# Optimization experiments

Measured on AMD Instinct MI355X. Metric: run time of the kernel, lower is better.

Reference implementation:

```python
import jax, jax.numpy as jnp
import numpy as np
import math

H = 1024   # d_model
NH = 32    # N // 2 state size
L_LEN = 4096
DT_MIN, DT_MAX = 0.001, 0.1


def setup_inputs() -> dict:
    key = jax.random.key(0)
    k1, k2, k3, k4 = jax.random.split(key, 4)
    C = jax.random.normal(k1, (H, NH, 2), dtype=jnp.float32)  # view_as_real complex C
    log_dt = (jax.random.uniform(k2, (H,), dtype=jnp.float32)
              * (math.log(DT_MAX) - math.log(DT_MIN)) + math.log(DT_MIN))
    # log of positive real parts (original: log(|Re(eig)|) repeated over H)
    log_A_real = jnp.log(0.5 + jax.random.uniform(k3, (H, NH), dtype=jnp.float32) * NH)
    A_imag = jax.random.normal(k4, (H, NH), dtype=jnp.float32) * math.pi
    return {"C": C, "log_dt": log_dt, "log_A_real": log_A_real,
            "A_imag": A_imag, "L": L_LEN}


def reference(C, log_dt, log_A_real, A_imag, L):
    dt = jnp.exp(log_dt)                                  # [H]
    Cc = C[..., 0] + 1j * C[..., 1]                       # [H, N] complex64
    A = -jnp.exp(log_A_real) - 1j * A_imag                # [H, N]
    dtA = A * dt[:, None]                                 # [H, N]
    # Vandermonde: exp(dtA)^l for l in [0, L)
    K = dtA[:, :, None] * jnp.arange(L, dtype=jnp.float32)  # [H, N, L]
    Cc = Cc * (jnp.exp(dtA) - 1.0) / A                    # [H, N]
    K = 2.0 * jnp.einsum('hn,hnl->hl', Cc, jnp.exp(K)).real  # [H, L]
    return K
```

## Files before the change

### kernel.cpp

```cpp
#include <hip/hip_runtime.h>
#include <math.h>


#define HH 1024
#define NH 32
#define LL 4096
#define BLOCK 256
#define CHUNK 4
#define SPLIT 4
#define STRIDE (BLOCK * SPLIT)

#define TWO_PI 6.28318530717958647692f
#define INV_TWO_PI 0.15915494309189533577f

__device__ __forceinline__ float sin_rev(float r) {
    float d;
    asm("v_sin_f32 %0, %1" : "=v"(d) : "v"(r));
    return d;
}
__device__ __forceinline__ float cos_rev(float r) {
    float d;
    asm("v_cos_f32 %0, %1" : "=v"(d) : "v"(r));
    return d;
}

__global__ __launch_bounds__(BLOCK) void s4_vandermonde(
    const float* __restrict__ C,
    const float* __restrict__ log_dt,
    const float* __restrict__ log_A_real,
    const float* __restrict__ A_imag,
    float* __restrict__ out)
{
    __shared__ float4 sA[NH];
    __shared__ float4 sB[NH];

    const int h = blockIdx.x >> 2;
    const int s = blockIdx.x & 3;
    const int t = threadIdx.x;

    if (t < NH) {
        const int n = t;
        const float dt  = __expf(log_dt[h]);
        const float Are = -__expf(log_A_real[h * NH + n]);
        const float Aim = -A_imag[h * NH + n];
        const float re = Are * dt;
        const float im = Aim * dt;
        float s1, c1;
        __sincosf(im, &s1, &c1);
        const float er1 = __expf(re);
        const float X = er1 * c1 - 1.0f;
        const float Y = er1 * s1;
        const float C0 = C[(h * NH + n) * 2 + 0];
        const float C1 = C[(h * NH + n) * 2 + 1];
        const float nr = C0 * X - C1 * Y;
        const float ni = C0 * Y + C1 * X;
        const float inv = 2.0f / (Are * Are + Aim * Aim);
        const float ctr = (nr * Are + ni * Aim) * inv;
        const float cti = (ni * Are - nr * Aim) * inv;
        const float fm = im * INV_TWO_PI;

        const float reS = re * (float)STRIDE;
        const float erS = (reS < -80.0f) ? 0.0f : __expf(reS);
        double revd = (double)fm * (double)STRIDE;
        revd -= floor(revd);
        float sS, cS;
        __sincosf((float)revd * TWO_PI, &sS, &cS);

        const float kl = -40.0f / (re * (float)STRIDE);
        const int kcap = (kl >= (float)(CHUNK - 1)) ? CHUNK : ((int)kl + 1);

        sA[n] = make_float4(ctr, cti, re, fm);
        sB[n] = make_float4(erS * cS, erS * sS, __int_as_float(kcap), 0.0f);
    }
    __syncthreads();

    float acc[CHUNK];
#pragma unroll
    for (int k = 0; k < CHUNK; ++k) acc[k] = 0.0f;

    const float lf = (float)(s * BLOCK + t);

    for (int n = 0; n < NH; ++n) {
        const float4 A4 = sA[n];
        const float a = A4.z * lf;
        if (a < -40.0f) continue;
        const float4 B4 = sB[n];
        const float er = __expf(a);
        float rev = A4.w * lf;
        rev -= floorf(rev);
        float zr = er * cos_rev(rev);
        float zi = er * sin_rev(rev);
        const int kcap = __float_as_int(B4.z);
#pragma unroll
        for (int k = 0; k < CHUNK; ++k) {
            if (k >= kcap) break;
            acc[k] += A4.x * zr - A4.y * zi;
            const float tr = zr * B4.x - zi * B4.y;
            zi = zr * B4.y + zi * B4.x;
            zr = tr;
        }
    }

    float* o = out + h * LL + s * BLOCK + t;
#pragma unroll
    for (int k = 0; k < CHUNK; ++k) o[k * STRIDE] = acc[k];
}

extern "C" void kernel_launch(void* const* d_in, const int* in_sizes, int n_in,
                              void* d_out, int out_size, void* d_ws, size_t ws_size,
                              hipStream_t stream) {
    const float* C          = (const float*)d_in[0];
    const float* log_dt     = (const float*)d_in[1];
    const float* log_A_real = (const float*)d_in[2];
    const float* A_imag     = (const float*)d_in[3];
    float* out              = (float*)d_out;

    s4_vandermonde<<<dim3(HH * SPLIT), dim3(BLOCK), 0, stream>>>(
        C, log_dt, log_A_real, A_imag, out);
}
```

Before: 86.83 us.

## Factor Vandermonde powers into shared-memory tables and use a real Chebyshev-style recurrence

Each block now precomputes per-state tables of z^e and C·z^(s*256+16e) in shared memory, using all threads, so the main loop builds z^l from one complex multiply of two table entries. This replaces the per-thread exp and sin/cos in the inner loop. The later powers at stride 1024 come from a second-order real recurrence (2Re(w)·u − |w|²·u_prev) rather than a full complex multiply. The per-n kcap early exit is replaced by a single skip threshold, and the extra barrier and table setup add a small fixed cost per block. Accuracy may drift slightly, because the factorised products and the recurrence accumulate rounding differently.

```diff
diff --git a/kernel.cpp b/kernel.cpp
--- a/kernel.cpp
+++ b/kernel.cpp
@@ -6,9 +6,8 @@
 #define NH 32
 #define LL 4096
 #define BLOCK 256
-#define CHUNK 4
 #define SPLIT 4
-#define STRIDE (BLOCK * SPLIT)
+#define STRIDE 1024
 
 #define TWO_PI 6.28318530717958647692f
 #define INV_TWO_PI 0.15915494309189533577f
@@ -31,8 +30,10 @@
     const float* __restrict__ A_imag,
     float* __restrict__ out)
 {
-    __shared__ float4 sA[NH];
-    __shared__ float4 sB[NH];
+    __shared__ float2 sW16[NH][16];
+    __shared__ float2 sW1[NH][16];
+    __shared__ float4 sP[NH];
+    __shared__ float4 sAux[NH];
 
     const int h = blockIdx.x >> 2;
     const int s = blockIdx.x & 3;
@@ -59,51 +60,71 @@
         const float cti = (ni * Are - nr * Aim) * inv;
         const float fm = im * INV_TWO_PI;
 
-        const float reS = re * (float)STRIDE;
-        const float erS = (reS < -80.0f) ? 0.0f : __expf(reS);
-        double revd = (double)fm * (double)STRIDE;
+        const float erS = __expf(re * 1024.0f);
+        double revd = (double)im * (double)INV_TWO_PI * 1024.0;
         revd -= floor(revd);
         float sS, cS;
         __sincosf((float)revd * TWO_PI, &sS, &cS);
 
-        const float kl = -40.0f / (re * (float)STRIDE);
-        const int kcap = (kl >= (float)(CHUNK - 1)) ? CHUNK : ((int)kl + 1);
-
-        sA[n] = make_float4(ctr, cti, re, fm);
-        sB[n] = make_float4(erS * cS, erS * sS, __int_as_float(kcap), 0.0f);
+        sP[n]   = make_float4(re, erS * cS, erS * sS, erS * erS);
+        sAux[n] = make_float4(fm, ctr, cti, re);
     }
     __syncthreads();
 
-    float acc[CHUNK];
+    {
+        const int n = t >> 3;
+        const int j = t & 7;
+        const float4 aux = sAux[n];
+        const float fm = aux.x, ctr = aux.y, cti = aux.z, re = aux.w;
 #pragma unroll
-    for (int k = 0; k < CHUNK; ++k) acc[k] = 0.0f;
+        for (int q = 0; q < 2; ++q) {
+            const int e = j + q * 8;
+            {
+                const float er = __expf(re * (float)e);
+                float rev = fm * (float)e;
+                rev -= floorf(rev);
+                sW1[n][e] = make_float2(er * cos_rev(rev), er * sin_rev(rev));
+            }
+            {
+                const float m = (float)(s * 256 + 16 * e);
+                const float er = __expf(re * m);
+                float rev = fm * m;
+                rev -= floorf(rev);
+                const float br = er * cos_rev(rev);
+                const float bi = er * sin_rev(rev);
+                sW16[n][e] = make_float2(ctr * br - cti * bi,
+                                         ctr * bi + cti * br);
+            }
+        }
+    }
+    __syncthreads();
 
+    float acc0 = 0.0f, acc1 = 0.0f, acc2 = 0.0f, acc3 = 0.0f;
     const float lf = (float)(s * BLOCK + t);
+    const int hi = t >> 4, lo = t & 15;
 
     for (int n = 0; n < NH; ++n) {
-        const float4 A4 = sA[n];
-        const float a = A4.z * lf;
-        if (a < -40.0f) continue;
-        const float4 B4 = sB[n];
-        const float er = __expf(a);
-        float rev = A4.w * lf;
-        rev -= floorf(rev);
-        float zr = er * cos_rev(rev);
-        float zi = er * sin_rev(rev);
-        const int kcap = __float_as_int(B4.z);
-#pragma unroll
-        for (int k = 0; k < CHUNK; ++k) {
-            if (k >= kcap) break;
-            acc[k] += A4.x * zr - A4.y * zi;
-            const float tr = zr * B4.x - zi * B4.y;
-            zi = zr * B4.y + zi * B4.x;
-            zr = tr;
-        }
+        const float4 P = sP[n];
+        if (P.x * lf < -16.0f) continue;
+        const float2 a2 = sW16[n][hi];
+        const float2 b2 = sW1[n][lo];
+        const float vr = a2.x * b2.x - a2.y * b2.y;
+        const float vi = a2.x * b2.y + a2.y * b2.x;
+        acc0 += vr;
+        const float u1 = vr * P.y - vi * P.z;
+        acc1 += u1;
+        const float aS = P.y + P.y;
+        const float u2 = aS * u1 - P.w * vr;
+        acc2 += u2;
+        const float u3 = aS * u2 - P.w * u1;
+        acc3 += u3;
     }
 
     float* o = out + h * LL + s * BLOCK + t;
-#pragma unroll
-    for (int k = 0; k < CHUNK; ++k) o[k * STRIDE] = acc[k];
+    o[0]          = acc0;
+    o[STRIDE]     = acc1;
+    o[2 * STRIDE] = acc2;
+    o[3 * STRIDE] = acc3;
 }
 
 extern "C" void kernel_launch(void* const* d_in, const int* in_sizes, int n_in,
```

Result: faster. 83.52 us (-3.8%).
